# Optimization experiments

Hardware: AMD Instinct MI355X
Metric: run time of the kernel (lower is better)

## Reference

```python
import jax, jax.numpy as jnp
import numpy as np
from itertools import combinations_with_replacement

B, T, F, L, POLY_ORDER = 16, 2048, 128, 16, 3


def _hilbert_filter(N):
    # Matches pytorch_hilbert: H[0]=0, H[1:N//2]=2, H[N//2]=0 (even N)
    h = np.zeros(N, dtype=np.float32)
    if N % 2 == 0:
        h[1:N // 2] = 2.0
    else:
        h[1:(N + 1) // 2] = 2.0
    return jnp.asarray(h)


def hilbert(sig, axis=1):
    N = sig.shape[axis]
    Xf = jnp.fft.fft(sig, axis=axis)
    shape = [1] * sig.ndim
    shape[axis] = N
    return jnp.fft.ifft(Xf * _hilbert_filter(N).reshape(shape), axis=axis)


def _combo_indices(latent, poly_order):
    # static index arrays, grouped by degree n
    return [np.array(list(combinations_with_replacement(range(latent), n)), dtype=np.int32)
            for n in range(1, poly_order + 1)]


def compute_library(z, poly_order):
    # z: [B, T, L] -> theta: [B, T, library_dim]
    feats = []
    for combos in _combo_indices(z.shape[-1], poly_order):
        zc = z[..., combos]            # [B, T, ncomb, n]
        feats.append(jnp.prod(zc, axis=-1))  # [B, T, ncomb]
    analytic = hilbert(z, axis=1)
    feats.append(z)
    feats.append(jnp.abs(analytic))    # extract_real_component
    feats.append(jnp.angle(analytic))  # extract_imaginary_component
    return jnp.concatenate(feats, axis=-1)


def setup_inputs() -> dict:
    key = jax.random.key(0)
    ks = jax.random.split(key, 7)
    lib_dim = L + 2 * L + sum(len(c) for c in _combo_indices(L, POLY_ORDER))
    s_enc = 1.0 / np.sqrt(F)
    s_dec = 1.0 / np.sqrt(L)
    s_sin = 1.0 / np.sqrt(lib_dim)
    return {
        "x": jax.random.normal(ks[0], (B, T, F), dtype=jnp.float32),
        "W_enc": jax.random.uniform(ks[1], (L, F), jnp.float32, -s_enc, s_enc),
        "b_enc": jax.random.uniform(ks[2], (L,), jnp.float32, -s_enc, s_enc),
        "W_dec": jax.random.uniform(ks[3], (F, L), jnp.float32, -s_dec, s_dec),
        "b_dec": jax.random.uniform(ks[4], (F,), jnp.float32, -s_dec, s_dec),
        "W_sindy": jax.random.uniform(ks[5], (L, lib_dim), jnp.float32, -s_sin, s_sin),
        "b_sindy": jax.random.uniform(ks[6], (L,), jnp.float32, -s_sin, s_sin),
    }


def reference(x, W_enc, b_enc, W_dec, b_dec, W_sindy, b_sindy):
    z = jnp.einsum('btf,lf->btl', x, W_enc) + b_enc          # encoder
    theta = compute_library(z, POLY_ORDER)                    # [B,T,lib_dim]
    y_hat = jnp.einsum('btd,ld->btl', theta, W_sindy) + b_sindy
    x_hat = jnp.einsum('btl,fl->btf', z, W_dec) + b_dec       # decoder
    # Jacobian of the linear encoder w.r.t. x is the constant weight matrix
    # broadcast per (b, t): identical math to the O((B*T)^2) autograd version.
    jac_z_x = jnp.broadcast_to(W_enc, (x.shape[0], x.shape[1], L, F))
    return (y_hat, x_hat, z, jac_z_x, W_sindy, W_dec)
```

## Files before the change

kernel.cpp:

```cpp
#include <hip/hip_runtime.h>
#include <math.h>

typedef unsigned short u16;
typedef unsigned int   u32;
typedef __attribute__((ext_vector_type(4))) float f32x4;

#define OFF_AT    0
#define OFF_PT    524288
#define OFF_WT    1048576
#define OFF_ZT    1064832
#define OFF_TWC   1589120
#define OFF_TWS   1591168

#define R1_LO 0
#define R1_HI 5592576
#define R23_LO 5592576
#define R23_HI 16777216

__device__ __forceinline__ void jac_range(const float* __restrict__ Wenc,
                                          float* __restrict__ out_jac,
                                          int lo, int hi, int idx, int nth)
{
    const float* wsrc = Wenc + (size_t)((lo + idx) & 511) * 4;
    f32x4 w;
    w.x = wsrc[0]; w.y = wsrc[1]; w.z = wsrc[2]; w.w = wsrc[3];
    f32x4* j4 = (f32x4*)out_jac;
    for (int i = lo + idx; i < hi; i += nth)
        __builtin_nontemporal_store(w, j4 + i);
}

__global__ __launch_bounds__(256) void k1_encdec(
    const float* __restrict__ x, const float* __restrict__ Wenc, const float* __restrict__ benc,
    const float* __restrict__ Wdec, const float* __restrict__ bdec,
    const float* __restrict__ Wsin,
    float* __restrict__ out_z, float* __restrict__ out_xhat,
    float* __restrict__ out_Ws, float* __restrict__ out_Wd,
    float* __restrict__ z_t, float* __restrict__ wt,
    double* __restrict__ twc_g, double* __restrict__ tws_g,
    float* __restrict__ out_jac)
{
    int tid = threadIdx.x;
    int blk = blockIdx.x;

    if (blk >= 1092) {
        jac_range(Wenc, out_jac, R1_LO, R1_HI, (blk - 1092) * 256 + tid, 262144);
        return;
    }
    if (blk >= 1024) {
        int t0 = (blk - 1024) * 256 + tid;
        if (t0 < 16256) {
            float v = Wsin[t0];
            out_Ws[t0] = v;
            int l = t0 / 1016;
            int d = t0 - l * 1016;
            if (d < 16) v += Wsin[t0 + 968];
            wt[d * 16 + l] = v;
        } else if (t0 < 17280) {
            int k = t0 - 16256;
            double ang = -6.283185307179586476925286766559 * (double)k / 2048.0;
            double s_, c_;
            sincos(ang, &s_, &c_);
            twc_g[k] = c_;
            tws_g[k] = s_;
        }
        if (t0 < 2048) out_Wd[t0] = Wdec[t0];
        return;
    }

    __shared__ float xs[32][132];
    __shared__ float we[16][132];
    __shared__ float wdT[16][132];
    __shared__ float zs[32][20];

    {
        const float4* xv = (const float4*)x + (size_t)blk * 1024;
        float4* xs4 = (float4*)&xs[0][0];
        #pragma unroll
        for (int h = 0; h < 4; ++h) {
            int vi = tid + h * 256;
            int pt = vi >> 5, fq = vi & 31;
            xs4[pt * 33 + fq] = xv[vi];
        }
    }
    {
        const float4* wev = (const float4*)Wenc;
        float4* we4 = (float4*)&we[0][0];
        #pragma unroll
        for (int h = 0; h < 2; ++h) {
            int vi = tid + h * 256;
            int l = vi >> 5, fq = vi & 31;
            we4[l * 33 + fq] = wev[vi];
        }
    }
    {
        const float4* wdv = (const float4*)Wdec;
        #pragma unroll
        for (int h = 0; h < 2; ++h) {
            int vi = tid + h * 256;
            float4 v = wdv[vi];
            int f = vi >> 2, lq = (vi & 3) * 4;
            wdT[lq + 0][f] = v.x; wdT[lq + 1][f] = v.y;
            wdT[lq + 2][f] = v.z; wdT[lq + 3][f] = v.w;
        }
    }
    __syncthreads();

    {
        int pt = tid >> 3, lp = tid & 7;
        const float4* xr = (const float4*)&xs[pt][0];
        const float4* wa = (const float4*)&we[lp][0];
        const float4* wb = (const float4*)&we[lp + 8][0];
        float s0 = 0.f, s1 = 0.f;
        #pragma unroll 8
        for (int fq = 0; fq < 32; ++fq) {
            float4 a = xr[fq], u = wa[fq], v = wb[fq];
            s0 = fmaf(a.x, u.x, s0); s0 = fmaf(a.y, u.y, s0);
            s0 = fmaf(a.z, u.z, s0); s0 = fmaf(a.w, u.w, s0);
            s1 = fmaf(a.x, v.x, s1); s1 = fmaf(a.y, v.y, s1);
            s1 = fmaf(a.z, v.z, s1); s1 = fmaf(a.w, v.w, s1);
        }
        zs[pt][lp]     = s0 + benc[lp];
        zs[pt][lp + 8] = s1 + benc[lp + 8];
    }
    __syncthreads();

    {
        #pragma unroll
        for (int h = 0; h < 2; ++h) {
            int i = tid + h * 256;
            out_z[(size_t)blk * 512 + i] = zs[i >> 4][i & 15];
        }
        #pragma unroll
        for (int h = 0; h < 2; ++h) {
            int i = tid + h * 256;
            int l = i >> 5, pt = i & 31;
            z_t[(size_t)l * 32768 + blk * 32 + pt] = zs[pt][l];
        }
    }

    {
        int f = tid & 127, half = tid >> 7;
        float w[16];
        #pragma unroll
        for (int l = 0; l < 16; ++l) w[l] = wdT[l][f];
        float bd = bdec[f];
        #pragma unroll
        for (int p = 0; p < 16; ++p) {
            int pt = half * 16 + p;
            const float4* zr = (const float4*)&zs[pt][0];
            float4 z0 = zr[0], z1 = zr[1], z2 = zr[2], z3 = zr[3];
            float acc = bd;
            acc = fmaf(z0.x, w[0],  acc); acc = fmaf(z0.y, w[1],  acc);
            acc = fmaf(z0.z, w[2],  acc); acc = fmaf(z0.w, w[3],  acc);
            acc = fmaf(z1.x, w[4],  acc); acc = fmaf(z1.y, w[5],  acc);
            acc = fmaf(z1.z, w[6],  acc); acc = fmaf(z1.w, w[7],  acc);
            acc = fmaf(z2.x, w[8],  acc); acc = fmaf(z2.y, w[9],  acc);
            acc = fmaf(z2.z, w[10], acc); acc = fmaf(z2.w, w[11], acc);
            acc = fmaf(z3.x, w[12], acc); acc = fmaf(z3.y, w[13], acc);
            acc = fmaf(z3.z, w[14], acc); acc = fmaf(z3.w, w[15], acc);
            out_xhat[(size_t)blk * 4096 + (size_t)pt * 128 + f] = acc;
        }
    }
}

#define TWPAD(k) ((k) + ((k) >> 5))
#define CP(i)    ((i) + ((i) >> 4))

#define EMIT2(EXPR) do {                                                    \
    if ((unsigned)(d - LO) < 121u) {                                        \
        float vv[2];                                                        \
        _Pragma("unroll") for (int p = 0; p < 2; ++p) vv[p] = (EXPR);       \
        int bb = (d - LO) << 4;                                             \
        _Pragma("unroll") for (int l = 0; l < 16; ++l) {                    \
            float w = lw[bb + l];                                           \
            acc[0][l] = fmaf(vv[0], w, acc[0][l]);                          \
            acc[1][l] = fmaf(vv[1], w, acc[1][l]);                          \
        }                                                                   \
    }                                                                       \
    ++d;                                                                    \
} while (0)

template<int LO>
__device__ __forceinline__ void poly_accum(const float (&z)[2][16],
                                           const float* __restrict__ lw,
                                           float (&acc)[2][16])
{
    int d = 0;
    #pragma unroll
    for (int i = 0; i < 16; ++i) EMIT2(z[p][i]);
    #pragma unroll
    for (int i = 0; i < 16; ++i)
        #pragma unroll
        for (int j = i; j < 16; ++j) EMIT2(z[p][i] * z[p][j]);
    #pragma unroll
    for (int i = 0; i < 16; ++i)
        #pragma unroll
        for (int j = i; j < 16; ++j)
            #pragma unroll
            for (int k = j; k < 16; ++k) EMIT2(z[p][i] * z[p][j] * z[p][k]);
}

__global__ __launch_bounds__(256, 2) void k23_fused(
    const float* __restrict__ z_t, const double* __restrict__ twc_g,
    const double* __restrict__ tws_g, const float* __restrict__ Wenc,
    const float* __restrict__ z_ws, const float* __restrict__ wt,
    float* __restrict__ a_t, float* __restrict__ p_t,
    float* __restrict__ part, float* __restrict__ out_jac)
{
    __shared__ float smem[6464];
    int tid = threadIdx.x;
    int blk = blockIdx.x;

    if (blk >= 768) {
        jac_range(Wenc, out_jac, R23_LO, R23_HI, (blk - 768) * 256 + tid, 393216);
        return;
    }

    if (blk < 256) {
        float2* c      = (float2*)smem;
        float*  twc_s  = smem + 4352;
        float*  tws_s  = smem + 5408;

        int b = blk >> 4, l = blk & 15;
        const size_t base = (size_t)l * 32768 + (size_t)b * 2048;
        const float* zp = z_t + base;

        #pragma unroll
        for (int h = 0; h < 4; ++h) {
            int k = tid + h * 256;
            twc_s[TWPAD(k)] = (float)twc_g[k];
            tws_s[TWPAD(k)] = (float)tws_g[k];
        }
        #pragma unroll
        for (int h = 0; h < 8; ++h) {
            int t = tid + h * 256;
            float2 v; v.x = zp[t]; v.y = 0.0f;
            c[CP(t)] = v;
        }
        __syncthreads();

        for (int half = 1024; half >= 1; half >>= 1) {
            int step = 1024 / half;
            #pragma unroll
            for (int h = 0; h < 4; ++h) {
                int t = tid + h * 256;
                int j = t & (half - 1);
                int pos = ((t - j) << 1) + j;
                int pa = CP(pos), pb = CP(pos + half);
                int ti = TWPAD(j * step);
                float2 u = c[pa], v = c[pb];
                float wc = twc_s[ti], wsn = tws_s[ti];
                float2 s, dsc;
                s.x = u.x + v.x;  s.y = u.y + v.y;
                float br = u.x - v.x, bi = u.y - v.y;
                dsc.x = br * wc - bi * wsn;
                dsc.y = br * wsn + bi * wc;
                c[pa] = s;
                c[pb] = dsc;
            }
            __syncthreads();
        }

        #pragma unroll
        for (int h = 0; h < 8; ++h) {
            int t = tid + h * 256;
            float sc = (t == 0 || (t & 1)) ? 0.0f : (2.0f / 2048.0f);
            int ci = CP(t);
            float2 v = c[ci];
            v.x *= sc; v.y *= sc;
            c[ci] = v;
        }
        __syncthreads();

        for (int half = 1; half <= 1024; half <<= 1) {
            int step = 1024 / half;
            #pragma unroll
            for (int h = 0; h < 4; ++h) {
                int t = tid + h * 256;
                int j = t & (half - 1);
                int pos = ((t - j) << 1) + j;
                int pa = CP(pos), pb = CP(pos + half);
                int ti = TWPAD(j * step);
                float2 u = c[pa], v = c[pb];
                float wc = twc_s[ti], wsn = tws_s[ti];
                float tr  = v.x * wc + v.y * wsn;
                float ti2 = v.y * wc - v.x * wsn;
                float2 p0, p1;
                p0.x = u.x + tr; p0.y = u.y + ti2;
                p1.x = u.x - tr; p1.y = u.y - ti2;
                c[pa] = p0;
                c[pb] = p1;
            }
            __syncthreads();
        }

        #pragma unroll
        for (int h = 0; h < 8; ++h) {
            int t = tid + h * 256;
            float2 v = c[CP(t)];
            a_t[base + t] = sqrtf(v.x * v.x + v.y * v.y);
            p_t[base + t] = atan2f(v.y, v.x);
        }
        return;
    }

    {
        float* lw = smem;
        int pb = blk - 256;
        int slice = pb >> 6;
        int ptgrp = pb & 63;
        int base = ptgrp * 512;

        {
            const float4* src = (const float4*)(wt + slice * 121 * 16);
            float4* dst = (float4*)lw;
            for (int i = tid; i < 484; i += 256) dst[i] = src[i];
        }
        __syncthreads();

        float z[2][16], acc[2][16];
        #pragma unroll
        for (int p = 0; p < 2; ++p) {
            int bt = base + p * 256 + tid;
            const float4* zp = (const float4*)(z_ws + (size_t)bt * 16);
            #pragma unroll
            for (int q = 0; q < 4; ++q) {
                float4 v = zp[q];
                z[p][q*4+0]=v.x; z[p][q*4+1]=v.y; z[p][q*4+2]=v.z; z[p][q*4+3]=v.w;
            }
        }
        #pragma unroll
        for (int p = 0; p < 2; ++p)
            #pragma unroll
            for (int l = 0; l < 16; ++l) acc[p][l] = 0.f;

        switch (slice) {
            case 0: poly_accum<0 * 121>(z, lw, acc); break;
            case 1: poly_accum<1 * 121>(z, lw, acc); break;
            case 2: poly_accum<2 * 121>(z, lw, acc); break;
            case 3: poly_accum<3 * 121>(z, lw, acc); break;
            case 4: poly_accum<4 * 121>(z, lw, acc); break;
            case 5: poly_accum<5 * 121>(z, lw, acc); break;
            case 6: poly_accum<6 * 121>(z, lw, acc); break;
            default: poly_accum<7 * 121>(z, lw, acc); break;
        }

        #pragma unroll
        for (int p = 0; p < 2; ++p) {
            int bt = base + p * 256 + tid;
            float4* pp = (float4*)(part + (size_t)slice * 524288 + (size_t)bt * 16);
            #pragma unroll
            for (int q = 0; q < 4; ++q) {
                float4 v;
                v.x = acc[p][q*4+0]; v.y = acc[p][q*4+1];
                v.z = acc[p][q*4+2]; v.w = acc[p][q*4+3];
                pp[q] = v;
            }
        }
    }
}

__global__ __launch_bounds__(256) void k3_tail(
    const float* __restrict__ part, const float* __restrict__ a_t,
    const float* __restrict__ p_t, const float* __restrict__ wt,
    const float* __restrict__ bsin, float* __restrict__ out_y)
{
    __shared__ float lw[512];
    int tid = threadIdx.x;
    if (tid < 128) {
        ((float4*)lw)[tid] = ((const float4*)(wt + 984 * 16))[tid];
    }
    __syncthreads();

    int bt = blockIdx.x * 128 + (tid >> 1);
    int lh = (tid & 1) * 8;
    float acc[8];
    {
        const float4* bp = (const float4*)bsin;
        #pragma unroll
        for (int q = 0; q < 2; ++q) {
            float4 v = bp[(lh >> 2) + q];
            acc[q*4+0]=v.x; acc[q*4+1]=v.y; acc[q*4+2]=v.z; acc[q*4+3]=v.w;
        }
    }
    #pragma unroll
    for (int sl = 0; sl < 8; ++sl) {
        const float4* pp = (const float4*)(part + (size_t)sl * 524288 + (size_t)bt * 16 + lh);
        #pragma unroll
        for (int q = 0; q < 2; ++q) {
            float4 v = pp[q];
            acc[q*4+0]+=v.x; acc[q*4+1]+=v.y; acc[q*4+2]+=v.z; acc[q*4+3]+=v.w;
        }
    }
    #pragma unroll
    for (int i = 0; i < 16; ++i) {
        float av = a_t[(size_t)i * 32768 + bt];
        #pragma unroll
        for (int l = 0; l < 8; ++l) acc[l] = fmaf(av, lw[i * 16 + lh + l], acc[l]);
    }
    #pragma unroll
    for (int i = 0; i < 16; ++i) {
        float pv = p_t[(size_t)i * 32768 + bt];
        #pragma unroll
        for (int l = 0; l < 8; ++l) acc[l] = fmaf(pv, lw[256 + i * 16 + lh + l], acc[l]);
    }

    float4* yp = (float4*)(out_y + (size_t)bt * 16 + lh);
    #pragma unroll
    for (int q = 0; q < 2; ++q) {
        float4 v;
        v.x = acc[q*4+0]; v.y = acc[q*4+1]; v.z = acc[q*4+2]; v.w = acc[q*4+3];
        yp[q] = v;
    }
}

extern "C" void kernel_launch(void* const* d_in, const int* in_sizes, int n_in,
                              void* d_out, int out_size, void* d_ws, size_t ws_size,
                              hipStream_t stream)
{
    const float* x  = (const float*)d_in[0];
    const float* We = (const float*)d_in[1];
    const float* be = (const float*)d_in[2];
    const float* Wd = (const float*)d_in[3];
    const float* bd = (const float*)d_in[4];
    const float* Ws = (const float*)d_in[5];
    const float* bs = (const float*)d_in[6];

    float* out  = (float*)d_out;
    float* o_y  = out;
    float* o_xh = out + 524288;
    float* o_z  = out + 4718592;
    float* o_j  = out + 5242880;
    float* o_Ws = out + 72351744;
    float* o_Wd = out + 72368000;

    float*  ws    = (float*)d_ws;
    float*  a_t   = ws + OFF_AT;
    float*  p_t   = ws + OFF_PT;
    float*  wt    = ws + OFF_WT;
    float*  z_t   = ws + OFF_ZT;
    double* twc_g = (double*)(ws + OFF_TWC);
    double* tws_g = (double*)(ws + OFF_TWS);
    float*  part  = ws + 1593216;

    hipLaunchKernelGGL(k1_encdec, dim3(2116), dim3(256), 0, stream,
                       x, We, be, Wd, bd, Ws, o_z, o_xh, o_Ws, o_Wd,
                       z_t, wt, twc_g, tws_g, o_j);
    hipLaunchKernelGGL(k23_fused, dim3(2304), dim3(256), 0, stream,
                       z_t, twc_g, tws_g, We, o_z, wt, a_t, p_t, part, o_j);
    hipLaunchKernelGGL(k3_tail, dim3(256), dim3(256), 0, stream,
                       part, a_t, p_t, wt, bs, o_y);
}
```

Baseline: 364.9 us.

## Fuse Hilbert transform into first kernel by recomputing z, rebalance jacobian stores

The Hilbert/FFT blocks move into the first kernel. Each block recomputes its z column directly from x and W_enc and computes its twiddle factors in-kernel, so the z_t and twiddle workspace round-trip is gone. The polynomial library kernel becomes its own launch. The constant jacobian broadcast store is split into three ranges spread across all three kernels. This trades redundant encoder work (each FFT block rereads a full batch of x) for removing a dependency stage, and it changes how the store-bound jacobian writes overlap with compute.

```diff
diff --git a/kernel.cpp b/kernel.cpp
--- a/kernel.cpp
+++ b/kernel.cpp
@@ -8,14 +8,13 @@
 #define OFF_AT    0
 #define OFF_PT    524288
 #define OFF_WT    1048576
-#define OFF_ZT    1064832
-#define OFF_TWC   1589120
-#define OFF_TWS   1591168
-
-#define R1_LO 0
-#define R1_HI 5592576
-#define R23_LO 5592576
-#define R23_HI 16777216
+
+#define RA_LO 0
+#define RA_HI 8388608
+#define RB_LO 8388608
+#define RB_HI 12582912
+#define RC_LO 12582912
+#define RC_HI 16777216
 
 __device__ __forceinline__ void jac_range(const float* __restrict__ Wenc,
                                           float* __restrict__ out_jac,
@@ -29,213 +28,69 @@
         __builtin_nontemporal_store(w, j4 + i);
 }
 
-__global__ __launch_bounds__(256) void k1_encdec(
+#define TWPAD(k) ((k) + ((k) >> 5))
+#define CP(i)    ((i) + ((i) >> 4))
+
+__global__ __launch_bounds__(256) void mega1(
     const float* __restrict__ x, const float* __restrict__ Wenc, const float* __restrict__ benc,
     const float* __restrict__ Wdec, const float* __restrict__ bdec,
     const float* __restrict__ Wsin,
     float* __restrict__ out_z, float* __restrict__ out_xhat,
     float* __restrict__ out_Ws, float* __restrict__ out_Wd,
-    float* __restrict__ z_t, float* __restrict__ wt,
-    double* __restrict__ twc_g, double* __restrict__ tws_g,
+    float* __restrict__ wt,
+    float* __restrict__ a_t, float* __restrict__ p_t,
     float* __restrict__ out_jac)
 {
+    __shared__ float smem[9088];
     int tid = threadIdx.x;
     int blk = blockIdx.x;
 
-    if (blk >= 1092) {
-        jac_range(Wenc, out_jac, R1_LO, R1_HI, (blk - 1092) * 256 + tid, 262144);
+    if (blk >= 1344) {
+        jac_range(Wenc, out_jac, RA_LO, RA_HI, (blk - 1344) * 256 + tid, 262144);
         return;
     }
-    if (blk >= 1024) {
-        int t0 = (blk - 1024) * 256 + tid;
-        if (t0 < 16256) {
-            float v = Wsin[t0];
-            out_Ws[t0] = v;
-            int l = t0 / 1016;
-            int d = t0 - l * 1016;
-            if (d < 16) v += Wsin[t0 + 968];
-            wt[d * 16 + l] = v;
-        } else if (t0 < 17280) {
-            int k = t0 - 16256;
+
+    if (blk >= 1088) {
+        float2* c     = (float2*)smem;
+        float*  twc_s = smem + 4352;
+        float*  tws_s = smem + 5408;
+        float*  weL   = smem + 6464;
+
+        int hb = blk - 1088;
+        int b = hb >> 4, l = hb & 15;
+        const size_t base = (size_t)l * 32768 + (size_t)b * 2048;
+
+        if (tid < 32) {
+            ((float4*)weL)[tid] = ((const float4*)Wenc)[l * 32 + tid];
+        }
+        #pragma unroll
+        for (int h = 0; h < 4; ++h) {
+            int k = tid + h * 256;
             double ang = -6.283185307179586476925286766559 * (double)k / 2048.0;
             double s_, c_;
             sincos(ang, &s_, &c_);
-            twc_g[k] = c_;
-            tws_g[k] = s_;
-        }
-        if (t0 < 2048) out_Wd[t0] = Wdec[t0];
-        return;
-    }
-
-    __shared__ float xs[32][132];
-    __shared__ float we[16][132];
-    __shared__ float wdT[16][132];
-    __shared__ float zs[32][20];
-
-    {
-        const float4* xv = (const float4*)x + (size_t)blk * 1024;
-        float4* xs4 = (float4*)&xs[0][0];
-        #pragma unroll
-        for (int h = 0; h < 4; ++h) {
-            int vi = tid + h * 256;
-            int pt = vi >> 5, fq = vi & 31;
-            xs4[pt * 33 + fq] = xv[vi];
-        }
-    }
-    {
-        const float4* wev = (const float4*)Wenc;
-        float4* we4 = (float4*)&we[0][0];
-        #pragma unroll
-        for (int h = 0; h < 2; ++h) {
-            int vi = tid + h * 256;
-            int l = vi >> 5, fq = vi & 31;
-            we4[l * 33 + fq] = wev[vi];
-        }
-    }
-    {
-        const float4* wdv = (const float4*)Wdec;
-        #pragma unroll
-        for (int h = 0; h < 2; ++h) {
-            int vi = tid + h * 256;
-            float4 v = wdv[vi];
-            int f = vi >> 2, lq = (vi & 3) * 4;
-            wdT[lq + 0][f] = v.x; wdT[lq + 1][f] = v.y;
-            wdT[lq + 2][f] = v.z; wdT[lq + 3][f] = v.w;
-        }
-    }
-    __syncthreads();
-
-    {
-        int pt = tid >> 3, lp = tid & 7;
-        const float4* xr = (const float4*)&xs[pt][0];
-        const float4* wa = (const float4*)&we[lp][0];
-        const float4* wb = (const float4*)&we[lp + 8][0];
-        float s0 = 0.f, s1 = 0.f;
-        #pragma unroll 8
-        for (int fq = 0; fq < 32; ++fq) {
-            float4 a = xr[fq], u = wa[fq], v = wb[fq];
-            s0 = fmaf(a.x, u.x, s0); s0 = fmaf(a.y, u.y, s0);
-            s0 = fmaf(a.z, u.z, s0); s0 = fmaf(a.w, u.w, s0);
-            s1 = fmaf(a.x, v.x, s1); s1 = fmaf(a.y, v.y, s1);
-            s1 = fmaf(a.z, v.z, s1); s1 = fmaf(a.w, v.w, s1);
-        }
-        zs[pt][lp]     = s0 + benc[lp];
-        zs[pt][lp + 8] = s1 + benc[lp + 8];
-    }
-    __syncthreads();
-
-    {
-        #pragma unroll
-        for (int h = 0; h < 2; ++h) {
-            int i = tid + h * 256;
-            out_z[(size_t)blk * 512 + i] = zs[i >> 4][i & 15];
-        }
-        #pragma unroll
-        for (int h = 0; h < 2; ++h) {
-            int i = tid + h * 256;
-            int l = i >> 5, pt = i & 31;
-            z_t[(size_t)l * 32768 + blk * 32 + pt] = zs[pt][l];
-        }
-    }
-
-    {
-        int f = tid & 127, half = tid >> 7;
-        float w[16];
-        #pragma unroll
-        for (int l = 0; l < 16; ++l) w[l] = wdT[l][f];
-        float bd = bdec[f];
-        #pragma unroll
-        for (int p = 0; p < 16; ++p) {
-            int pt = half * 16 + p;
-            const float4* zr = (const float4*)&zs[pt][0];
-            float4 z0 = zr[0], z1 = zr[1], z2 = zr[2], z3 = zr[3];
-            float acc = bd;
-            acc = fmaf(z0.x, w[0],  acc); acc = fmaf(z0.y, w[1],  acc);
-            acc = fmaf(z0.z, w[2],  acc); acc = fmaf(z0.w, w[3],  acc);
-            acc = fmaf(z1.x, w[4],  acc); acc = fmaf(z1.y, w[5],  acc);
-            acc = fmaf(z1.z, w[6],  acc); acc = fmaf(z1.w, w[7],  acc);
-            acc = fmaf(z2.x, w[8],  acc); acc = fmaf(z2.y, w[9],  acc);
-            acc = fmaf(z2.z, w[10], acc); acc = fmaf(z2.w, w[11], acc);
-            acc = fmaf(z3.x, w[12], acc); acc = fmaf(z3.y, w[13], acc);
-            acc = fmaf(z3.z, w[14], acc); acc = fmaf(z3.w, w[15], acc);
-            out_xhat[(size_t)blk * 4096 + (size_t)pt * 128 + f] = acc;
-        }
-    }
-}
-
-#define TWPAD(k) ((k) + ((k) >> 5))
-#define CP(i)    ((i) + ((i) >> 4))
-
-#define EMIT2(EXPR) do {                                                    \
-    if ((unsigned)(d - LO) < 121u) {                                        \
-        float vv[2];                                                        \
-        _Pragma("unroll") for (int p = 0; p < 2; ++p) vv[p] = (EXPR);       \
-        int bb = (d - LO) << 4;                                             \
-        _Pragma("unroll") for (int l = 0; l < 16; ++l) {                    \
-            float w = lw[bb + l];                                           \
-            acc[0][l] = fmaf(vv[0], w, acc[0][l]);                          \
-            acc[1][l] = fmaf(vv[1], w, acc[1][l]);                          \
-        }                                                                   \
-    }                                                                       \
-    ++d;                                                                    \
-} while (0)
-
-template<int LO>
-__device__ __forceinline__ void poly_accum(const float (&z)[2][16],
-                                           const float* __restrict__ lw,
-                                           float (&acc)[2][16])
-{
-    int d = 0;
-    #pragma unroll
-    for (int i = 0; i < 16; ++i) EMIT2(z[p][i]);
-    #pragma unroll
-    for (int i = 0; i < 16; ++i)
-        #pragma unroll
-        for (int j = i; j < 16; ++j) EMIT2(z[p][i] * z[p][j]);
-    #pragma unroll
-    for (int i = 0; i < 16; ++i)
-        #pragma unroll
-        for (int j = i; j < 16; ++j)
+            twc_s[TWPAD(k)] = (float)c_;
+            tws_s[TWPAD(k)] = (float)s_;
+        }
+        __syncthreads();
+
+        {
+            float bl = benc[l];
             #pragma unroll
-            for (int k = j; k < 16; ++k) EMIT2(z[p][i] * z[p][j] * z[p][k]);
-}
-
-__global__ __launch_bounds__(256, 2) void k23_fused(
-    const float* __restrict__ z_t, const double* __restrict__ twc_g,
-    const double* __restrict__ tws_g, const float* __restrict__ Wenc,
-    const float* __restrict__ z_ws, const float* __restrict__ wt,
-    float* __restrict__ a_t, float* __restrict__ p_t,
-    float* __restrict__ part, float* __restrict__ out_jac)
-{
-    __shared__ float smem[6464];
-    int tid = threadIdx.x;
-    int blk = blockIdx.x;
-
-    if (blk >= 768) {
-        jac_range(Wenc, out_jac, R23_LO, R23_HI, (blk - 768) * 256 + tid, 393216);
-        return;
-    }
-
-    if (blk < 256) {
-        float2* c      = (float2*)smem;
-        float*  twc_s  = smem + 4352;
-        float*  tws_s  = smem + 5408;
-
-        int b = blk >> 4, l = blk & 15;
-        const size_t base = (size_t)l * 32768 + (size_t)b * 2048;
-        const float* zp = z_t + base;
-
-        #pragma unroll
-        for (int h = 0; h < 4; ++h) {
-            int k = tid + h * 256;
-            twc_s[TWPAD(k)] = (float)twc_g[k];
-            tws_s[TWPAD(k)] = (float)tws_g[k];
-        }
-        #pragma unroll
-        for (int h = 0; h < 8; ++h) {
-            int t = tid + h * 256;
-            float2 v; v.x = zp[t]; v.y = 0.0f;
-            c[CP(t)] = v;
+            for (int h = 0; h < 8; ++h) {
+                int t = tid + h * 256;
+                const float4* xr = (const float4*)x + ((size_t)b * 2048 + t) * 32;
+                const float4* wr = (const float4*)weL;
+                float s = 0.f;
+                #pragma unroll 8
+                for (int fq = 0; fq < 32; ++fq) {
+                    float4 a = xr[fq], w = wr[fq];
+                    s = fmaf(a.x, w.x, s); s = fmaf(a.y, w.y, s);
+                    s = fmaf(a.z, w.z, s); s = fmaf(a.w, w.w, s);
+                }
+                float2 v; v.x = s + bl; v.y = 0.0f;
+                c[CP(t)] = v;
+            }
         }
         __syncthreads();
 
@@ -304,58 +159,203 @@
         return;
     }
 
-    {
-        float* lw = smem;
-        int pb = blk - 256;
-        int slice = pb >> 6;
-        int ptgrp = pb & 63;
-        int base = ptgrp * 512;
-
-        {
-            const float4* src = (const float4*)(wt + slice * 121 * 16);
-            float4* dst = (float4*)lw;
-            for (int i = tid; i < 484; i += 256) dst[i] = src[i];
-        }
-        __syncthreads();
-
-        float z[2][16], acc[2][16];
-        #pragma unroll
-        for (int p = 0; p < 2; ++p) {
-            int bt = base + p * 256 + tid;
-            const float4* zp = (const float4*)(z_ws + (size_t)bt * 16);
+    if (blk >= 1024) {
+        int t0 = (blk - 1024) * 256 + tid;
+        if (t0 < 16256) {
+            float v = Wsin[t0];
+            out_Ws[t0] = v;
+            int l = t0 / 1016;
+            int d = t0 - l * 1016;
+            if (d < 16) v += Wsin[t0 + 968];
+            wt[d * 16 + l] = v;
+        }
+        if (t0 < 2048) out_Wd[t0] = Wdec[t0];
+        return;
+    }
+
+    float* xs  = smem;
+    float* we  = smem + 4224;
+    float* wdT = smem + 6336;
+    float* zs  = smem + 8448;
+
+    {
+        const float4* xv = (const float4*)x + (size_t)blk * 1024;
+        float4* xs4 = (float4*)xs;
+        #pragma unroll
+        for (int h = 0; h < 4; ++h) {
+            int vi = tid + h * 256;
+            int pt = vi >> 5, fq = vi & 31;
+            xs4[pt * 33 + fq] = xv[vi];
+        }
+    }
+    {
+        const float4* wev = (const float4*)Wenc;
+        float4* we4 = (float4*)we;
+        #pragma unroll
+        for (int h = 0; h < 2; ++h) {
+            int vi = tid + h * 256;
+            int l = vi >> 5, fq = vi & 31;
+            we4[l * 33 + fq] = wev[vi];
+        }
+    }
+    {
+        const float4* wdv = (const float4*)Wdec;
+        #pragma unroll
+        for (int h = 0; h < 2; ++h) {
+            int vi = tid + h * 256;
+            float4 v = wdv[vi];
+            int f = vi >> 2, lq = (vi & 3) * 4;
+            wdT[(lq + 0) * 132 + f] = v.x; wdT[(lq + 1) * 132 + f] = v.y;
+            wdT[(lq + 2) * 132 + f] = v.z; wdT[(lq + 3) * 132 + f] = v.w;
+        }
+    }
+    __syncthreads();
+
+    {
+        int pt = tid >> 3, lp = tid & 7;
+        const float4* xr = (const float4*)(xs + pt * 132);
+        const float4* wa = (const float4*)(we + lp * 132);
+        const float4* wb = (const float4*)(we + (lp + 8) * 132);
+        float s0 = 0.f, s1 = 0.f;
+        #pragma unroll 8
+        for (int fq = 0; fq < 32; ++fq) {
+            float4 a = xr[fq], u = wa[fq], v = wb[fq];
+            s0 = fmaf(a.x, u.x, s0); s0 = fmaf(a.y, u.y, s0);
+            s0 = fmaf(a.z, u.z, s0); s0 = fmaf(a.w, u.w, s0);
+            s1 = fmaf(a.x, v.x, s1); s1 = fmaf(a.y, v.y, s1);
+            s1 = fmaf(a.z, v.z, s1); s1 = fmaf(a.w, v.w, s1);
+        }
+        zs[pt * 20 + lp]     = s0 + benc[lp];
+        zs[pt * 20 + lp + 8] = s1 + benc[lp + 8];
+    }
+    __syncthreads();
+
+    {
+        #pragma unroll
+        for (int h = 0; h < 2; ++h) {
+            int i = tid + h * 256;
+            out_z[(size_t)blk * 512 + i] = zs[(i >> 4) * 20 + (i & 15)];
+        }
+    }
+
+    {
+        int f = tid & 127, half = tid >> 7;
+        float w[16];
+        #pragma unroll
+        for (int l = 0; l < 16; ++l) w[l] = wdT[l * 132 + f];
+        float bd = bdec[f];
+        #pragma unroll
+        for (int p = 0; p < 16; ++p) {
+            int pt = half * 16 + p;
+            const float4* zr = (const float4*)(zs + pt * 20);
+            float4 z0 = zr[0], z1 = zr[1], z2 = zr[2], z3 = zr[3];
+            float acc = bd;
+            acc = fmaf(z0.x, w[0],  acc); acc = fmaf(z0.y, w[1],  acc);
+            acc = fmaf(z0.z, w[2],  acc); acc = fmaf(z0.w, w[3],  acc);
+            acc = fmaf(z1.x, w[4],  acc); acc = fmaf(z1.y, w[5],  acc);
+            acc = fmaf(z1.z, w[6],  acc); acc = fmaf(z1.w, w[7],  acc);
+            acc = fmaf(z2.x, w[8],  acc); acc = fmaf(z2.y, w[9],  acc);
+            acc = fmaf(z2.z, w[10], acc); acc = fmaf(z2.w, w[11], acc);
+            acc = fmaf(z3.x, w[12], acc); acc = fmaf(z3.y, w[13], acc);
+            acc = fmaf(z3.z, w[14], acc); acc = fmaf(z3.w, w[15], acc);
+            out_xhat[(size_t)blk * 4096 + (size_t)pt * 128 + f] = acc;
+        }
+    }
+}
+
+#define EMIT2(EXPR) do {                                                    \
+    if ((unsigned)(d - LO) < 121u) {                                        \
+        float vv[2];                                                        \
+        _Pragma("unroll") for (int p = 0; p < 2; ++p) vv[p] = (EXPR);       \
+        int bb = (d - LO) << 4;                                             \
+        _Pragma("unroll") for (int l = 0; l < 16; ++l) {                    \
+            float w = lw[bb + l];                                           \
+            acc[0][l] = fmaf(vv[0], w, acc[0][l]);                          \
+            acc[1][l] = fmaf(vv[1], w, acc[1][l]);                          \
+        }                                                                   \
+    }                                                                       \
+    ++d;                                                                    \
+} while (0)
+
+template<int LO>
+__device__ __forceinline__ void poly_accum(const float (&z)[2][16],
+                                           const float* __restrict__ lw,
+                                           float (&acc)[2][16])
+{
+    int d = 0;
+    #pragma unroll
+    for (int i = 0; i < 16; ++i) EMIT2(z[p][i]);
+    #pragma unroll
+    for (int i = 0; i < 16; ++i)
+        #pragma unroll
+        for (int j = i; j < 16; ++j) EMIT2(z[p][i] * z[p][j]);
+    #pragma unroll
+    for (int i = 0; i < 16; ++i)
+        #pragma unroll
+        for (int j = i; j < 16; ++j)
             #pragma unroll
-            for (int q = 0; q < 4; ++q) {
-                float4 v = zp[q];
-                z[p][q*4+0]=v.x; z[p][q*4+1]=v.y; z[p][q*4+2]=v.z; z[p][q*4+3]=v.w;
-            }
-        }
-        #pragma unroll
-        for (int p = 0; p < 2; ++p)
-            #pragma unroll
-            for (int l = 0; l < 16; ++l) acc[p][l] = 0.f;
-
-        switch (slice) {
-            case 0: poly_accum<0 * 121>(z, lw, acc); break;
-            case 1: poly_accum<1 * 121>(z, lw, acc); break;
-            case 2: poly_accum<2 * 121>(z, lw, acc); break;
-            case 3: poly_accum<3 * 121>(z, lw, acc); break;
-            case 4: poly_accum<4 * 121>(z, lw, acc); break;
-            case 5: poly_accum<5 * 121>(z, lw, acc); break;
-            case 6: poly_accum<6 * 121>(z, lw, acc); break;
-            default: poly_accum<7 * 121>(z, lw, acc); break;
-        }
-
-        #pragma unroll
-        for (int p = 0; p < 2; ++p) {
-            int bt = base + p * 256 + tid;
-            float4* pp = (float4*)(part + (size_t)slice * 524288 + (size_t)bt * 16);
-            #pragma unroll
-            for (int q = 0; q < 4; ++q) {
-                float4 v;
-                v.x = acc[p][q*4+0]; v.y = acc[p][q*4+1];
-                v.z = acc[p][q*4+2]; v.w = acc[p][q*4+3];
-                pp[q] = v;
-            }
+            for (int k = j; k < 16; ++k) EMIT2(z[p][i] * z[p][j] * z[p][k]);
+}
+
+__global__ __launch_bounds__(256, 2) void k3_yhat(
+    const float* __restrict__ z_ws, const float* __restrict__ wt,
+    const float* __restrict__ Wenc,
+    float* __restrict__ part, float* __restrict__ out_jac)
+{
+    __shared__ float lw[1936];
+    int tid = threadIdx.x;
+    if (blockIdx.x >= 512) {
+        jac_range(Wenc, out_jac, RB_LO, RB_HI, (blockIdx.x - 512) * 256 + tid, 131072);
+        return;
+    }
+    int slice = blockIdx.x >> 6;
+    int ptgrp = blockIdx.x & 63;
+    int base = ptgrp * 512;
+
+    {
+        const float4* src = (const float4*)(wt + slice * 121 * 16);
+        float4* dst = (float4*)lw;
+        for (int i = tid; i < 484; i += 256) dst[i] = src[i];
+    }
+    __syncthreads();
+
+    float z[2][16], acc[2][16];
+    #pragma unroll
+    for (int p = 0; p < 2; ++p) {
+        int bt = base + p * 256 + tid;
+        const float4* zp = (const float4*)(z_ws + (size_t)bt * 16);
+        #pragma unroll
+        for (int q = 0; q < 4; ++q) {
+            float4 v = zp[q];
+            z[p][q*4+0]=v.x; z[p][q*4+1]=v.y; z[p][q*4+2]=v.z; z[p][q*4+3]=v.w;
+        }
+    }
+    #pragma unroll
+    for (int p = 0; p < 2; ++p)
+        #pragma unroll
+        for (int l = 0; l < 16; ++l) acc[p][l] = 0.f;
+
+    switch (slice) {
+        case 0: poly_accum<0 * 121>(z, lw, acc); break;
+        case 1: poly_accum<1 * 121>(z, lw, acc); break;
+        case 2: poly_accum<2 * 121>(z, lw, acc); break;
+        case 3: poly_accum<3 * 121>(z, lw, acc); break;
+        case 4: poly_accum<4 * 121>(z, lw, acc); break;
+        case 5: poly_accum<5 * 121>(z, lw, acc); break;
+        case 6: poly_accum<6 * 121>(z, lw, acc); break;
+        default: poly_accum<7 * 121>(z, lw, acc); break;
+    }
+
+    #pragma unroll
+    for (int p = 0; p < 2; ++p) {
+        int bt = base + p * 256 + tid;
+        float4* pp = (float4*)(part + (size_t)slice * 524288 + (size_t)bt * 16);
+        #pragma unroll
+        for (int q = 0; q < 4; ++q) {
+            float4 v;
+            v.x = acc[p][q*4+0]; v.y = acc[p][q*4+1];
+            v.z = acc[p][q*4+2]; v.w = acc[p][q*4+3];
+            pp[q] = v;
         }
     }
 }
@@ -363,10 +363,15 @@
 __global__ __launch_bounds__(256) void k3_tail(
     const float* __restrict__ part, const float* __restrict__ a_t,
     const float* __restrict__ p_t, const float* __restrict__ wt,
-    const float* __restrict__ bsin, float* __restrict__ out_y)
+    const float* __restrict__ bsin, const float* __restrict__ Wenc,
+    float* __restrict__ out_y, float* __restrict__ out_jac)
 {
     __shared__ float lw[512];
     int tid = threadIdx.x;
+    if (blockIdx.x >= 256) {
+        jac_range(Wenc, out_jac, RC_LO, RC_HI, (blockIdx.x - 256) * 256 + tid, 131072);
+        return;
+    }
     if (tid < 128) {
         ((float4*)lw)[tid] = ((const float4*)(wt + 984 * 16))[tid];
     }
@@ -438,16 +443,13 @@
     float*  a_t   = ws + OFF_AT;
     float*  p_t   = ws + OFF_PT;
     float*  wt    = ws + OFF_WT;
-    float*  z_t   = ws + OFF_ZT;
-    double* twc_g = (double*)(ws + OFF_TWC);
-    double* tws_g = (double*)(ws + OFF_TWS);
     float*  part  = ws + 1593216;
 
-    hipLaunchKernelGGL(k1_encdec, dim3(2116), dim3(256), 0, stream,
+    hipLaunchKernelGGL(mega1, dim3(2368), dim3(256), 0, stream,
                        x, We, be, Wd, bd, Ws, o_z, o_xh, o_Ws, o_Wd,
-                       z_t, wt, twc_g, tws_g, o_j);
-    hipLaunchKernelGGL(k23_fused, dim3(2304), dim3(256), 0, stream,
-                       z_t, twc_g, tws_g, We, o_z, wt, a_t, p_t, part, o_j);
-    hipLaunchKernelGGL(k3_tail, dim3(256), dim3(256), 0, stream,
-                       part, a_t, p_t, wt, bs, o_y);
-}
+                       wt, a_t, p_t, o_j);
+    hipLaunchKernelGGL(k3_yhat, dim3(1024), dim3(256), 0, stream,
+                       o_z, wt, We, part, o_j);
+    hipLaunchKernelGGL(k3_tail, dim3(768), dim3(256), 0, stream,
+                       part, a_t, p_t, wt, bs, We, o_y, o_j);
+}
```

Measured after the change: 383.2 us. +5.0%, slower.
